# Performance work log

Measured on AMD Instinct MI355X. Metric: run time of the kernel, lower is better.

## Reference

```python
import jax, jax.numpy as jnp
import numpy as np

NUM_GROUPS = 32
EPS = 1e-6


def setup_inputs() -> dict:
    key = jax.random.key(0)
    ks = jax.random.split(key, 10)
    B, C, L = 8, 512, 4096
    s = 1.0 / np.sqrt(C)
    x = jax.random.normal(ks[0], (B, C, L), dtype=jnp.float32)
    gn_w = jnp.ones((C,), jnp.float32)
    gn_b = jnp.zeros((C,), jnp.float32)
    wq = jax.random.normal(ks[1], (C, C), jnp.float32) * s
    bq = jax.random.normal(ks[2], (C,), jnp.float32) * 0.01
    wk = jax.random.normal(ks[3], (C, C), jnp.float32) * s
    bk = jax.random.normal(ks[4], (C,), jnp.float32) * 0.01
    wv = jax.random.normal(ks[5], (C, C), jnp.float32) * s
    bv = jax.random.normal(ks[6], (C,), jnp.float32) * 0.01
    wo = jax.random.normal(ks[7], (C, C), jnp.float32) * s
    bo = jax.random.normal(ks[8], (C,), jnp.float32) * 0.01
    return {"x": x, "gn_w": gn_w, "gn_b": gn_b, "wq": wq, "bq": bq,
            "wk": wk, "bk": bk, "wv": wv, "bv": bv, "wo": wo, "bo": bo}


def _group_norm(x, w, b):
    # x: [B, C, L]; normalize over each group's (C/G, L) slice
    B, C, L = x.shape
    g = x.reshape(B, NUM_GROUPS, C // NUM_GROUPS, L)
    mu = jnp.mean(g, axis=(2, 3), keepdims=True)
    var = jnp.var(g, axis=(2, 3), keepdims=True)
    g = (g - mu) * jax.lax.rsqrt(var + EPS)
    return g.reshape(B, C, L) * w[None, :, None] + b[None, :, None]


def _conv1x1(h, w, b):
    # pointwise conv: [B,C,L] x [Cout,Cin] -> [B,Cout,L]
    return jnp.einsum('oc,bcl->bol', w, h) + b[None, :, None]


def reference(x, gn_w, gn_b, wq, bq, wk, bk, wv, bv, wo, bo):
    h = _group_norm(x, gn_w, gn_b)
    q = _conv1x1(h, wq, bq)
    k = _conv1x1(h, wk, bk)
    v = _conv1x1(h, wv, bv)
    B, C, L = q.shape
    scale = jnp.asarray(C, q.dtype) ** -0.5
    # w_[b,i,j] = sum_c q[b,c,i] k[b,c,j]
    w_ = jnp.einsum('bci,bcj->bij', q, k) * scale
    w_ = jax.nn.softmax(w_, axis=2)
    # h[b,c,i] = sum_j v[b,c,j] w_[b,i,j]
    h = jnp.einsum('bcj,bij->bci', v, w_)
    return x + _conv1x1(h, wo, bo)
```

## Files before the change

### kernel.cpp

```cpp
#include <hip/hip_runtime.h>
#include <hip/hip_bf16.h>
#include <math.h>

#define DI __device__ __forceinline__

typedef unsigned short u16;
typedef unsigned int   u32;
typedef unsigned long long u64;
typedef __attribute__((ext_vector_type(8))) short short8;
typedef __attribute__((ext_vector_type(4))) float f32x4;

constexpr int CB = 512;
constexpr int LL = 4096;
constexpr int NG = 32;

DI float bf2f(u16 u) { u32 v = ((u32)u) << 16; float f; __builtin_memcpy(&f, &v, 4); return f; }
DI u16 f2bf(float f) {
  u32 u; __builtin_memcpy(&u, &f, 4);
  u += 0x7fffu + ((u >> 16) & 1u);
  return (u16)(u >> 16);
}

DI void gload16(const void* g, void* l) {
  __builtin_amdgcn_global_load_lds((const __attribute__((address_space(1))) u32*)g,
                                   (__attribute__((address_space(3))) u32*)l, 16, 0, 0);
}

__global__ __launch_bounds__(256) void conv_w(
    const float* __restrict__ wq, const float* __restrict__ wk,
    const float* __restrict__ wv, const float* __restrict__ wo,
    const float* __restrict__ bq, const float* __restrict__ bk,
    const float* __restrict__ bv,
    u16* __restrict__ wqkv, u16* __restrict__ wob, float* __restrict__ bqkv) {
  if (blockIdx.x < 1024) {
    int i = blockIdx.x * 256 + threadIdx.x;
    wqkv[i]          = f2bf(wq[i]);
    wqkv[262144 + i] = f2bf(wk[i]);
    wqkv[524288 + i] = f2bf(wv[i]);
    wob[i]           = f2bf(wo[i]);
  } else {
    for (int j = 0; j < 6; ++j) {
      int idx = j * 256 + threadIdx.x;
      float b = (idx < 512) ? bq[idx] : (idx < 1024) ? bk[idx - 512] : bv[idx - 1024];
      bqkv[idx] = b;
    }
  }
}

__global__ __launch_bounds__(256) void gn_stats(const float* __restrict__ x,
                                                float* __restrict__ stats) {
  const float4* base = (const float4*)(x + (long)blockIdx.x * (16 * LL));
  float s = 0.f, ss = 0.f;
  for (int i = threadIdx.x; i < 16 * LL / 4; i += 256) {
    float4 v = base[i];
    s  += v.x + v.y + v.z + v.w;
    ss += v.x * v.x + v.y * v.y + v.z * v.z + v.w * v.w;
  }
#pragma unroll
  for (int o = 32; o; o >>= 1) { s += __shfl_xor(s, o); ss += __shfl_xor(ss, o); }
  __shared__ float red[8];
  int wv = threadIdx.x >> 6, ln = threadIdx.x & 63;
  if (ln == 0) { red[wv * 2] = s; red[wv * 2 + 1] = ss; }
  __syncthreads();
  if (threadIdx.x == 0) {
    float S = red[0] + red[2] + red[4] + red[6];
    float SS = red[1] + red[3] + red[5] + red[7];
    float mu = S * (1.f / 65536.f);
    float var = SS * (1.f / 65536.f) - mu * mu;
    stats[blockIdx.x * 2]     = mu;
    stats[blockIdx.x * 2 + 1] = rsqrtf(var + 1e-6f);
  }
}

__global__ __launch_bounds__(256) void gn_apply(
    const float* __restrict__ x, const float* __restrict__ gw,
    const float* __restrict__ gb, const float* __restrict__ stats,
    u16* __restrict__ hT) {
  __shared__ u16 t[64][66];
  const int b = blockIdx.z, c0 = blockIdx.y * 64, l0 = blockIdx.x * 64;
  const int ln = threadIdx.x & 63, sub = threadIdx.x >> 6;
  for (int cr = sub; cr < 64; cr += 4) {
    int c = c0 + cr;
    float v  = x[(long)b * CB * LL + (long)c * LL + l0 + ln];
    float mu = stats[(b * NG + (c >> 4)) * 2];
    float rs = stats[(b * NG + (c >> 4)) * 2 + 1];
    t[cr][ln] = f2bf((v - mu) * rs * gw[c] + gb[c]);
  }
  __syncthreads();
  for (int lr = sub; lr < 64; lr += 4)
    hT[(long)b * LL * CB + (long)(l0 + lr) * CB + c0 + ln] = t[ln][lr];
}

template <int BM, int BN, int EPI, bool SWZ, int WR, int WC>
__global__ __launch_bounds__(WR * WC * 64) void gemm_bt(
    const u16* __restrict__ A, int lda, long asb,
    const u16* __restrict__ Bt, int ldb, long bsb,
    int K, const float* __restrict__ bias, float scale,
    u16* __restrict__ o0, u16* __restrict__ o1, u16* __restrict__ o2,
    float* __restrict__ of, const float* __restrict__ xres, long osb, int ldo) {
  constexpr int NT = WR * WC * 64;
  constexpr int FM = BM / WR / 16, FN = BN / WC / 16;
  static_assert((BM * 8) % NT == 0 && (BN * 8) % NT == 0, "staging div");
  __shared__ u16 smem[(BM + BN) * 64];
  u16* lA = smem;
  u16* lB = smem + BM * 64;

  int bx = blockIdx.x, by = blockIdx.y;
  if constexpr (SWZ) {
    const int nwg = gridDim.x * gridDim.y;
    const int id = by * gridDim.x + bx;
    const int id2 = (id & 7) * (nwg >> 3) + (id >> 3);
    bx = id2 % gridDim.x;
    by = id2 / gridDim.x;
  }

  const int tid = threadIdx.x;
  const int lane = tid & 63;
  const int wv = tid >> 6;
  const int wr = wv / WC, wc = wv % WC;
  const int fr = lane & 15, fq = lane >> 4;
  const int bz = blockIdx.z;
  const int bzb  = (EPI == 4) ? (bz >> 1) : bz;
  const int kbeg = (EPI == 4) ? (bz & 1) * K : 0;

  const u16* Ab = A + (long)bzb * asb + (long)(by * BM) * lda;
  const u16* Bb = Bt + (long)bzb * bsb + (long)(bx * BN) * ldb;

  f32x4 acc[FM][FN];
#pragma unroll
  for (int m = 0; m < FM; ++m)
#pragma unroll
    for (int n = 0; n < FN; ++n) acc[m][n] = (f32x4)(0.f);

  for (int k0 = kbeg; k0 < kbeg + K; k0 += 64) {
#pragma unroll
    for (int p = 0; p < BM * 8 / NT; ++p) {
      int t = p * NT + tid;
      int row = t >> 3;
      int cbl = ((t & 7) << 4) ^ ((row & 7) << 4);
      gload16(Ab + (long)row * lda + k0 + (cbl >> 1), &lA[t * 8]);
    }
#pragma unroll
    for (int p = 0; p < BN * 8 / NT; ++p) {
      int t = p * NT + tid;
      int row = t >> 3;
      int cbl = ((t & 7) << 4) ^ ((row & 7) << 4);
      gload16(Bb + (long)row * ldb + k0 + (cbl >> 1), &lB[t * 8]);
    }
    __syncthreads();
#pragma unroll
    for (int ks = 0; ks < 2; ++ks) {
      short8 af[FM], bfr[FN];
#pragma unroll
      for (int m = 0; m < FM; ++m) {
        int row = wr * (BM / WR) + m * 16 + fr;
        int cb = (ks * 64 + fq * 16) ^ ((row & 7) << 4);
        af[m] = *(const short8*)((const char*)lA + row * 128 + cb);
      }
#pragma unroll
      for (int n = 0; n < FN; ++n) {
        int row = wc * (BN / WC) + n * 16 + fr;
        int cb = (ks * 64 + fq * 16) ^ ((row & 7) << 4);
        bfr[n] = *(const short8*)((const char*)lB + row * 128 + cb);
      }
#pragma unroll
      for (int m = 0; m < FM; ++m)
#pragma unroll
        for (int n = 0; n < FN; ++n)
          acc[m][n] = __builtin_amdgcn_mfma_f32_16x16x32_bf16(af[m], bfr[n], acc[m][n], 0, 0, 0);
    }
    __syncthreads();
  }

  const int ml0 = wr * (BM / WR);
  const int nl0 = wc * (BN / WC);

  if constexpr (EPI == 3) {
    const int mg0 = by * BM + ml0;
    const int ng0 = bx * BN + nl0;
#pragma unroll
    for (int m = 0; m < FM; ++m)
#pragma unroll
      for (int n = 0; n < FN; ++n) {
        const int ng = ng0 + n * 16 + fr;
#pragma unroll
        for (int r = 0; r < 4; ++r) {
          const int mg = mg0 + m * 16 + fq * 4 + r;
          const long off = (long)bz * osb + (long)mg * ldo + ng;
          of[off] = acc[m][n][r] + bias[mg] + xres[off];
        }
      }
  } else if constexpr (EPI == 0) {
    const int mat = (by * BM) >> 9;
    if (mat < 2) {
#pragma unroll
      for (int m = 0; m < FM; ++m)
#pragma unroll
        for (int n = 0; n < FN; ++n) {
          const int nl = nl0 + n * 16 + fr;
#pragma unroll
          for (int r = 0; r < 4; ++r) {
            const int ml = ml0 + m * 16 + fq * 4 + r;
            smem[nl * BM + (ml ^ ((nl & 7) << 3))] =
                f2bf(acc[m][n][r] + bias[by * BM + ml]);
          }
        }
      __syncthreads();
      u16* dst0 = (mat == 0 ? o0 : o1) + (long)bz * ((long)LL * CB) +
                  (long)(bx * BN) * CB + ((by * BM) & 511);
      for (int i = tid * 8; i < BM * BN; i += NT * 8) {
        const int rr = i / BM, cc = i % BM;
        short8 val = *(const short8*)&smem[rr * BM + (cc ^ ((rr & 7) << 3))];
        *(short8*)(dst0 + (long)rr * CB + cc) = val;
      }
    } else {
#pragma unroll
      for (int m = 0; m < FM; ++m)
#pragma unroll
        for (int n = 0; n < FN; ++n) {
          const int nl = nl0 + n * 16 + fr;
#pragma unroll
          for (int r = 0; r < 4; ++r) {
            const int ml = ml0 + m * 16 + fq * 4 + r;
            smem[ml * BN + (nl ^ ((ml & 7) << 3))] =
                f2bf(acc[m][n][r] + bias[by * BM + ml]);
          }
        }
      __syncthreads();
      u16* dst0 = o2 + (long)bz * ((long)CB * LL) +
                  (long)((by * BM) & 511) * LL + bx * BN;
      for (int i = tid * 8; i < BM * BN; i += NT * 8) {
        const int rr = i / BN, cc = i % BN;
        short8 val = *(const short8*)&smem[rr * BN + (cc ^ ((rr & 7) << 3))];
        *(short8*)(dst0 + (long)rr * LL + cc) = val;
      }
    }
  } else if constexpr (EPI == 4) {
#pragma unroll
    for (int m = 0; m < FM; ++m)
#pragma unroll
      for (int n = 0; n < FN; ++n) {
        const int nl = nl0 + n * 16 + fr;
#pragma unroll
        for (int r = 0; r < 4; ++r) {
          const int ml = ml0 + m * 16 + fq * 4 + r;
          smem[ml * BN + (nl ^ ((ml & 7) << 3))] = f2bf(acc[m][n][r]);
        }
      }
    __syncthreads();
    u16* dst0 = ((bz & 1) ? o1 : o0) + (long)(bz >> 1) * ((long)LL * CB) +
                (long)(by * BM) * ldo + bx * BN;
    for (int i = tid * 8; i < BM * BN; i += NT * 8) {
      const int rr = i / BN, cc = i % BN;
      short8 val = *(const short8*)&smem[rr * BN + (cc ^ ((rr & 7) << 3))];
      *(short8*)(dst0 + (long)rr * ldo + cc) = val;
    }
  } else {
#pragma unroll
    for (int m = 0; m < FM; ++m)
#pragma unroll
      for (int n = 0; n < FN; ++n) {
        const int nl = nl0 + n * 16 + fr;
#pragma unroll
        for (int r = 0; r < 4; ++r) {
          const int ml = ml0 + m * 16 + fq * 4 + r;
          smem[ml * BN + (nl ^ ((ml & 7) << 3))] = f2bf(acc[m][n][r] * scale);
        }
      }
    __syncthreads();
    u16* dst0 = o0 + (long)bz * osb + (long)(by * BM) * ldo + bx * BN;
    for (int i = tid * 8; i < BM * BN; i += NT * 8) {
      const int rr = i / BN, cc = i % BN;
      short8 val = *(const short8*)&smem[rr * BN + (cc ^ ((rr & 7) << 3))];
      *(short8*)(dst0 + (long)rr * ldo + cc) = val;
    }
  }
}

__global__ __launch_bounds__(256) void softmax_row(u16* __restrict__ S) {
  u16* row = S + ((long)blockIdx.y * LL + blockIdx.x) * LL;
  const int tid = threadIdx.x;
  const int wv = tid >> 6, ln = tid & 63;
  short8 a = ((const short8*)row)[tid * 2];
  short8 b = ((const short8*)row)[tid * 2 + 1];
  float v[16];
#pragma unroll
  for (int j = 0; j < 8; ++j) { v[j] = bf2f((u16)a[j]); v[8 + j] = bf2f((u16)b[j]); }
  float mx = -1e30f;
#pragma unroll
  for (int j = 0; j < 16; ++j) mx = fmaxf(mx, v[j]);
#pragma unroll
  for (int o = 32; o; o >>= 1) mx = fmaxf(mx, __shfl_xor(mx, o));
  __shared__ float red[4];
  if (ln == 0) red[wv] = mx;
  __syncthreads();
  mx = fmaxf(fmaxf(red[0], red[1]), fmaxf(red[2], red[3]));
  __syncthreads();
  float sum = 0.f;
#pragma unroll
  for (int j = 0; j < 16; ++j) { v[j] = __expf(v[j] - mx); sum += v[j]; }
#pragma unroll
  for (int o = 32; o; o >>= 1) sum += __shfl_xor(sum, o);
  if (ln == 0) red[wv] = sum;
  __syncthreads();
  sum = red[0] + red[1] + red[2] + red[3];
  const float r = 1.f / sum;
  short8 o1, o2;
#pragma unroll
  for (int j = 0; j < 8; ++j) { o1[j] = (short)f2bf(v[j] * r); o2[j] = (short)f2bf(v[8 + j] * r); }
  ((short8*)row)[tid * 2] = o1;
  ((short8*)row)[tid * 2 + 1] = o2;
}

__global__ __launch_bounds__(256) void reduce_pp(
    const u16* __restrict__ p0, const u16* __restrict__ p1, u16* __restrict__ o) {
  const long base = (long)blockIdx.y * ((long)LL * CB) +
                    (long)(blockIdx.x * 256 + threadIdx.x) * 16;
#pragma unroll
  for (int h = 0; h < 2; ++h) {
    short8 a = *(const short8*)(p0 + base + h * 8);
    short8 b = *(const short8*)(p1 + base + h * 8);
    short8 r;
#pragma unroll
    for (int j = 0; j < 8; ++j)
      r[j] = (short)f2bf(bf2f((u16)a[j]) + bf2f((u16)b[j]));
    *(short8*)(o + base + h * 8) = r;
  }
}

extern "C" void kernel_launch(void* const* d_in, const int* in_sizes, int n_in,
                              void* d_out, int out_size, void* d_ws, size_t ws_size,
                              hipStream_t stream) {
  const float* x   = (const float*)d_in[0];
  const float* gnw = (const float*)d_in[1];
  const float* gnb = (const float*)d_in[2];
  const float* wq  = (const float*)d_in[3];
  const float* bq  = (const float*)d_in[4];
  const float* wk  = (const float*)d_in[5];
  const float* bk  = (const float*)d_in[6];
  const float* wv  = (const float*)d_in[7];
  const float* bv  = (const float*)d_in[8];
  const float* wo  = (const float*)d_in[9];
  const float* bo  = (const float*)d_in[10];
  float* out = (float*)d_out;

  char* ws = (char*)d_ws;
  const long NEL = (long)LL * CB;
  const long SEL = (long)LL * LL;
  float* stats = (float*)ws;
  float* bqkv  = (float*)(ws + 8192);
  u16* wqkv = (u16*)(ws + 16384);
  u16* wob  = (u16*)(ws + 16384 + 1572864);
  u16* hT   = (u16*)(ws + (4l << 20));
  u16* qT   = hT + 8 * NEL;
  u16* kT   = qT + 8 * NEL;
  u16* vN   = kT + 8 * NEL;
  const size_t base = (4ul << 20) + 4ul * 8 * NEL * 2;

  int G;
  u16 *Sbuf, *aT;
  if (ws_size >= base + 2ul * SEL * 2) G = 2;
  else                                 G = 1;
  if (G > 1) { Sbuf = (u16*)(ws + base); aT = hT; }
  else       { Sbuf = hT; aT = qT; }

  conv_w<<<1025, 256, 0, stream>>>(wq, wk, wv, wo, bq, bk, bv, wqkv, wob, bqkv);
  gn_stats<<<256, 256, 0, stream>>>(x, stats);
  gn_apply<<<dim3(64, 8, 8), 256, 0, stream>>>(x, gnw, gnb, stats, hT);

  gemm_bt<128, 128, 0, true, 2, 2><<<dim3(32, 12, 8), 256, 0, stream>>>(
      wqkv, 512, 0, hT, 512, NEL, 512, bqkv, 1.f, qT, kT, vN, nullptr, nullptr, 0, 0);

  const float scal = 1.0f / sqrtf(512.0f);
  for (int g0 = 0; g0 < 8; g0 += G) {
    gemm_bt<128, 128, 1, true, 2, 2><<<dim3(32, 32, G), 256, 0, stream>>>(
        qT + (long)g0 * NEL, 512, NEL, kT + (long)g0 * NEL, 512, NEL, 512,
        nullptr, scal, Sbuf, nullptr, nullptr, nullptr, nullptr, SEL, LL);
    softmax_row<<<dim3(LL, G), 256, 0, stream>>>(Sbuf);
    if (G == 2) {
      gemm_bt<128, 128, 4, true, 2, 4><<<dim3(4, 32, 4), 512, 0, stream>>>(
          Sbuf, LL, SEL, vN + (long)g0 * NEL, LL, NEL, 2048,
          nullptr, 1.f, qT + (long)g0 * NEL, kT + (long)g0 * NEL, nullptr,
          nullptr, nullptr, 0, CB);
      reduce_pp<<<dim3(512, 2), 256, 0, stream>>>(
          qT + (long)g0 * NEL, kT + (long)g0 * NEL, aT + (long)g0 * NEL);
    } else {
      gemm_bt<128, 64, 2, true, 2, 2><<<dim3(8, 32, 1), 256, 0, stream>>>(
          Sbuf, LL, 0, vN + (long)g0 * NEL, LL, 0, LL,
          nullptr, 1.f, aT + (long)g0 * NEL, nullptr, nullptr, nullptr, nullptr, NEL, CB);
    }
  }

  gemm_bt<128, 128, 3, true, 2, 2><<<dim3(32, 4, 8), 256, 0, stream>>>(
      wob, 512, 0, aT, 512, NEL, 512, bo, 1.f,
      nullptr, nullptr, nullptr, out, x, NEL, LL);

  (void)in_sizes; (void)n_in; (void)out_size; (void)ws_size;
}
```

Baseline: 687.7 us.

## Fuse exp into score GEMM and defer softmax normalization to PV epilogue

The score GEMM epilogue now writes exp2 of the log2e-scaled scores directly. The softmax kernel becomes a read-only row-sum pass that stores reciprocal row sums. The PV GEMM multiplies its partial results by those reciprocals, and the split-K PV path is now used for both G settings. This removes the write-back of the normalized score matrix and one full pass of exp work, but drops the max subtraction, so large scores could overflow. It also flips a template boolean on several GEMMs.

```diff
diff --git a/kernel.cpp b/kernel.cpp
--- a/kernel.cpp
+++ b/kernel.cpp
@@ -236,6 +236,7 @@
       }
     }
   } else if constexpr (EPI == 4) {
+    const float* rls = xres + (long)(bz >> 1) * LL + by * BM;
 #pragma unroll
     for (int m = 0; m < FM; ++m)
 #pragma unroll
@@ -244,7 +245,7 @@
 #pragma unroll
         for (int r = 0; r < 4; ++r) {
           const int ml = ml0 + m * 16 + fq * 4 + r;
-          smem[ml * BN + (nl ^ ((ml & 7) << 3))] = f2bf(acc[m][n][r]);
+          smem[ml * BN + (nl ^ ((ml & 7) << 3))] = f2bf(acc[m][n][r] * rls[ml]);
         }
       }
     __syncthreads();
@@ -264,7 +265,7 @@
 #pragma unroll
         for (int r = 0; r < 4; ++r) {
           const int ml = ml0 + m * 16 + fq * 4 + r;
-          smem[ml * BN + (nl ^ ((ml & 7) << 3))] = f2bf(acc[m][n][r] * scale);
+          smem[ml * BN + (nl ^ ((ml & 7) << 3))] = f2bf(exp2f(acc[m][n][r] * scale));
         }
       }
     __syncthreads();
@@ -277,39 +278,24 @@
   }
 }
 
-__global__ __launch_bounds__(256) void softmax_row(u16* __restrict__ S) {
-  u16* row = S + ((long)blockIdx.y * LL + blockIdx.x) * LL;
+__global__ __launch_bounds__(256) void rsum_rows(const u16* __restrict__ S,
+                                                 float* __restrict__ rls) {
+  const u16* row = S + ((long)blockIdx.y * LL + blockIdx.x) * LL;
   const int tid = threadIdx.x;
   const int wv = tid >> 6, ln = tid & 63;
   short8 a = ((const short8*)row)[tid * 2];
   short8 b = ((const short8*)row)[tid * 2 + 1];
-  float v[16];
-#pragma unroll
-  for (int j = 0; j < 8; ++j) { v[j] = bf2f((u16)a[j]); v[8 + j] = bf2f((u16)b[j]); }
-  float mx = -1e30f;
-#pragma unroll
-  for (int j = 0; j < 16; ++j) mx = fmaxf(mx, v[j]);
-#pragma unroll
-  for (int o = 32; o; o >>= 1) mx = fmaxf(mx, __shfl_xor(mx, o));
+  float s = 0.f;
+#pragma unroll
+  for (int j = 0; j < 8; ++j) s += bf2f((u16)a[j]) + bf2f((u16)b[j]);
+#pragma unroll
+  for (int o = 32; o; o >>= 1) s += __shfl_xor(s, o);
   __shared__ float red[4];
-  if (ln == 0) red[wv] = mx;
+  if (ln == 0) red[wv] = s;
   __syncthreads();
-  mx = fmaxf(fmaxf(red[0], red[1]), fmaxf(red[2], red[3]));
-  __syncthreads();
-  float sum = 0.f;
-#pragma unroll
-  for (int j = 0; j < 16; ++j) { v[j] = __expf(v[j] - mx); sum += v[j]; }
-#pragma unroll
-  for (int o = 32; o; o >>= 1) sum += __shfl_xor(sum, o);
-  if (ln == 0) red[wv] = sum;
-  __syncthreads();
-  sum = red[0] + red[1] + red[2] + red[3];
-  const float r = 1.f / sum;
-  short8 o1, o2;
-#pragma unroll
-  for (int j = 0; j < 8; ++j) { o1[j] = (short)f2bf(v[j] * r); o2[j] = (short)f2bf(v[8 + j] * r); }
-  ((short8*)row)[tid * 2] = o1;
-  ((short8*)row)[tid * 2 + 1] = o2;
+  if (tid == 0)
+    rls[(long)blockIdx.y * LL + blockIdx.x] =
+        1.0f / (red[0] + red[1] + red[2] + red[3]);
 }
 
 __global__ __launch_bounds__(256) void reduce_pp(
@@ -351,6 +337,7 @@
   float* bqkv  = (float*)(ws + 8192);
   u16* wqkv = (u16*)(ws + 16384);
   u16* wob  = (u16*)(ws + 16384 + 1572864);
+  float* rlsm = (float*)(ws + (3l << 20));
   u16* hT   = (u16*)(ws + (4l << 20));
   u16* qT   = hT + 8 * NEL;
   u16* kT   = qT + 8 * NEL;
@@ -368,30 +355,24 @@
   gn_stats<<<256, 256, 0, stream>>>(x, stats);
   gn_apply<<<dim3(64, 8, 8), 256, 0, stream>>>(x, gnw, gnb, stats, hT);
 
-  gemm_bt<128, 128, 0, true, 2, 2><<<dim3(32, 12, 8), 256, 0, stream>>>(
+  gemm_bt<128, 128, 0, false, 2, 2><<<dim3(32, 12, 8), 256, 0, stream>>>(
       wqkv, 512, 0, hT, 512, NEL, 512, bqkv, 1.f, qT, kT, vN, nullptr, nullptr, 0, 0);
 
-  const float scal = 1.0f / sqrtf(512.0f);
+  const float cl = (1.0f / sqrtf(512.0f)) * 1.44269504f;
   for (int g0 = 0; g0 < 8; g0 += G) {
-    gemm_bt<128, 128, 1, true, 2, 2><<<dim3(32, 32, G), 256, 0, stream>>>(
+    gemm_bt<128, 128, 1, false, 2, 2><<<dim3(32, 32, G), 256, 0, stream>>>(
         qT + (long)g0 * NEL, 512, NEL, kT + (long)g0 * NEL, 512, NEL, 512,
-        nullptr, scal, Sbuf, nullptr, nullptr, nullptr, nullptr, SEL, LL);
-    softmax_row<<<dim3(LL, G), 256, 0, stream>>>(Sbuf);
-    if (G == 2) {
-      gemm_bt<128, 128, 4, true, 2, 4><<<dim3(4, 32, 4), 512, 0, stream>>>(
-          Sbuf, LL, SEL, vN + (long)g0 * NEL, LL, NEL, 2048,
-          nullptr, 1.f, qT + (long)g0 * NEL, kT + (long)g0 * NEL, nullptr,
-          nullptr, nullptr, 0, CB);
-      reduce_pp<<<dim3(512, 2), 256, 0, stream>>>(
-          qT + (long)g0 * NEL, kT + (long)g0 * NEL, aT + (long)g0 * NEL);
-    } else {
-      gemm_bt<128, 64, 2, true, 2, 2><<<dim3(8, 32, 1), 256, 0, stream>>>(
-          Sbuf, LL, 0, vN + (long)g0 * NEL, LL, 0, LL,
-          nullptr, 1.f, aT + (long)g0 * NEL, nullptr, nullptr, nullptr, nullptr, NEL, CB);
-    }
-  }
-
-  gemm_bt<128, 128, 3, true, 2, 2><<<dim3(32, 4, 8), 256, 0, stream>>>(
+        nullptr, cl, Sbuf, nullptr, nullptr, nullptr, nullptr, SEL, LL);
+    rsum_rows<<<dim3(LL, G), 256, 0, stream>>>(Sbuf, rlsm);
+    gemm_bt<128, 128, 4, true, 2, 4><<<dim3(4, 32, 2 * G), 512, 0, stream>>>(
+        Sbuf, LL, SEL, vN + (long)g0 * NEL, LL, NEL, 2048,
+        nullptr, 1.f, qT + (long)g0 * NEL, kT + (long)g0 * NEL, nullptr,
+        nullptr, rlsm, 0, CB);
+    reduce_pp<<<dim3(512, G), 256, 0, stream>>>(
+        qT + (long)g0 * NEL, kT + (long)g0 * NEL, aT + (long)g0 * NEL);
+  }
+
+  gemm_bt<128, 128, 3, false, 2, 2><<<dim3(32, 4, 8), 256, 0, stream>>>(
       wob, 512, 0, aT, 512, NEL, 512, bo, 1.f,
       nullptr, nullptr, nullptr, out, x, NEL, LL);
 
```

After: 627.6 us. 1.1x faster.
